# Kernel optimization log

Hardware: AMD Instinct MI355X
Metric: run time of the kernel (lower is better)

The kernel has to match this reference:

```python
import jax, jax.numpy as jnp
import numpy as np

N_SITES = 16
BATCH = 8192
K = 256
EPS = 1e-10


def _entanglement_entropy(sites_A, sites_B):
    # sites_A: [b, pA, k], sites_B: [b, pB, k]
    corr = jnp.einsum('bik,bjk->bij', sites_A, sites_B)  # [b, pA, pB]
    s = jnp.linalg.svd(corr, compute_uv=False)           # [b, min(pA,pB)]
    s_sq = s * s + EPS
    p = s_sq / jnp.sum(s_sq, axis=-1, keepdims=True)
    return -jnp.sum(p * jnp.log(p + EPS), axis=-1)        # [b]


def setup_inputs() -> dict:
    key = jax.random.key(0)
    sites = jax.random.normal(key, (BATCH, N_SITES, K), dtype=jnp.float32)
    return {"sites": sites}


def reference(sites) -> jnp.ndarray:
    # sites: [batch, n_sites, k]; list-of-tensors in the original, stacked here.
    n = sites.shape[1]
    mid = n // 2  # 8
    # Whole-system bipartition
    S_whole = _entanglement_entropy(sites[:, :mid], sites[:, mid:])
    # Left half bipartition (mid_left = mid // 2 = 4)
    ml = mid // 2
    S_left = _entanglement_entropy(sites[:, :ml], sites[:, ml:mid])
    # Right half bipartition
    nr = n - mid
    mr = nr // 2
    S_right = _entanglement_entropy(sites[:, mid:mid + mr], sites[:, mid + mr:])
    phi_q = S_whole - (S_left + S_right)
    return jax.nn.relu(phi_q)
```

## Files before the change

kernel.cpp:

```cpp
#include <hip/hip_runtime.h>
#include <math.h>

#define DEV __device__ __forceinline__

DEV float rcp_fast(float x) { return __builtin_amdgcn_rcpf(x); }
DEV float rsq_fast(float x) { return __builtin_amdgcn_rsqf(x); }

__host__ __device__ constexpr int TI(int n, int i, int j) {
  return n * i - (i * (i - 1)) / 2 + (j - i);
}

template <int N>
DEV float& sym_at(float (&a)[N * (N + 1) / 2], int i, int j) {
  return (i <= j) ? a[TI(N, i, j)] : a[TI(N, j, i)];
}

template <int N, int SWEEPS>
DEV void jacobi_sweeps(float (&a)[N * (N + 1) / 2]) {
  float tr = 0.0f;
#pragma unroll
  for (int i = 0; i < N; ++i) tr += a[TI(N, i, i)];
  const float thr = fabsf(tr) * 1e-8f + 1e-30f;
  for (int sw = 0; sw < SWEEPS; ++sw) {
#pragma unroll
    for (int p = 0; p < N - 1; ++p) {
#pragma unroll
      for (int q = p + 1; q < N; ++q) {
        float apq = a[TI(N, p, q)];
        if (fabsf(apq) > thr) {
          float app = a[TI(N, p, p)];
          float aqq = a[TI(N, q, q)];
          float h  = aqq - app;
          float tw = apq + apq;
          float den = fabsf(h) + sqrtf(fmaf(h, h, tw * tw));
          float t = tw * rcp_fast(den);
          t = (h < 0.0f) ? -t : t;
          float c = rsq_fast(fmaf(t, t, 1.0f));
          float s = t * c;
          float tau = s * rcp_fast(1.0f + c);
          a[TI(N, p, p)] = fmaf(-t, apq, app);
          a[TI(N, q, q)] = fmaf( t, apq, aqq);
          a[TI(N, p, q)] = 0.0f;
#pragma unroll
          for (int i = 0; i < N; ++i) {
            if (i != p && i != q) {
              float g  = sym_at<N>(a, i, p);
              float hh = sym_at<N>(a, i, q);
              sym_at<N>(a, i, p) = fmaf(-s, fmaf( tau, g, hh), g);
              sym_at<N>(a, i, q) = fmaf( s, fmaf(-tau, hh, g), hh);
            }
          }
        }
      }
    }
  }
}

template <int N>
DEV float entropy_of(const float (&a)[N * (N + 1) / 2]) {
  float lam[N];
  float sum = 0.0f;
#pragma unroll
  for (int i = 0; i < N; ++i) {
    float l = fmaxf(a[TI(N, i, i)], 0.0f) + 1e-10f;
    lam[i] = l;
    sum += l;
  }
  float inv = 1.0f / sum;
  float H = 0.0f;
#pragma unroll
  for (int i = 0; i < N; ++i) {
    float p = lam[i] * inv;
    H = fmaf(p, __logf(p + 1e-10f), H);
  }
  return -H;
}

DEV float reduce_dist_64(float (&cur)[64], int lane) {
#pragma unroll
  for (int d = 0; d < 6; ++d) {
    const int dist = 1 << d;
    const int up = (lane >> d) & 1;
#pragma unroll
    for (int m = 0; m < (64 >> (d + 1)); ++m) {
      float snd = up ? cur[2 * m]     : cur[2 * m + 1];
      float kp  = up ? cur[2 * m + 1] : cur[2 * m];
      float r = __shfl_xor(snd, dist, 64);
      cur[m] = kp + r;
    }
  }
  return cur[0];
}

DEV float reduce_dist_32(float (&cur)[32], int lane) {
#pragma unroll
  for (int d = 0; d < 5; ++d) {
    const int dist = 1 << d;
    const int up = (lane >> d) & 1;
#pragma unroll
    for (int m = 0; m < (32 >> (d + 1)); ++m) {
      float snd = up ? cur[2 * m]     : cur[2 * m + 1];
      float kp  = up ? cur[2 * m + 1] : cur[2 * m];
      float r = __shfl_xor(snd, dist, 64);
      cur[m] = kp + r;
    }
  }
  float v = cur[0];
  v += __shfl_xor(v, 32, 64);
  return v;
}

__global__ __launch_bounds__(64) void corr_kernel(
    const float* __restrict__ sites, float* __restrict__ cmat) {
  const int b = blockIdx.x;
  const int lane = threadIdx.x;
  const float4* base = reinterpret_cast<const float4*>(sites) + (size_t)b * 1024;

  float4 v[16];
#pragma unroll
  for (int s = 0; s < 16; ++s) v[s] = base[s * 64 + lane];

  float aw[64];
#pragma unroll
  for (int i = 0; i < 8; ++i) {
#pragma unroll
    for (int j = 0; j < 8; ++j) {
      float4 a = v[i], c = v[8 + j];
      aw[i * 8 + j] =
          fmaf(a.x, c.x, fmaf(a.y, c.y, fmaf(a.z, c.z, a.w * c.w)));
    }
  }
  float cw = reduce_dist_64(aw, lane);

  float alr[32];
#pragma unroll
  for (int i = 0; i < 4; ++i) {
#pragma unroll
    for (int j = 0; j < 4; ++j) {
      float4 a = v[i], c = v[4 + j];
      alr[i * 4 + j] =
          fmaf(a.x, c.x, fmaf(a.y, c.y, fmaf(a.z, c.z, a.w * c.w)));
      float4 a2 = v[8 + i], c2 = v[12 + j];
      alr[16 + i * 4 + j] =
          fmaf(a2.x, c2.x, fmaf(a2.y, c2.y, fmaf(a2.z, c2.z, a2.w * c2.w)));
    }
  }
  float clr = reduce_dist_32(alr, lane);

  cmat[(size_t)lane * 8192 + b] = cw;
  if (lane < 32) cmat[(size_t)(64 + lane) * 8192 + b] = clr;
}

__global__ __launch_bounds__(64) void phi_kernel(
    const float* __restrict__ cmat, float* __restrict__ out) {
  const int b = blockIdx.x * 64 + threadIdx.x;

  float Cw[64];
#pragma unroll
  for (int e = 0; e < 64; ++e) Cw[e] = cmat[(size_t)e * 8192 + b];
  float Mw[36];
#pragma unroll
  for (int i = 0; i < 8; ++i) {
#pragma unroll
    for (int j = i; j < 8; ++j) {
      float acc = 0.0f;
#pragma unroll
      for (int k = 0; k < 8; ++k) acc = fmaf(Cw[i * 8 + k], Cw[j * 8 + k], acc);
      Mw[TI(8, i, j)] = acc;
    }
  }
  jacobi_sweeps<8, 6>(Mw);
  float Sw = entropy_of<8>(Mw);

  float Cl[16];
#pragma unroll
  for (int e = 0; e < 16; ++e) Cl[e] = cmat[(size_t)(64 + e) * 8192 + b];
  float Ml[10];
#pragma unroll
  for (int i = 0; i < 4; ++i) {
#pragma unroll
    for (int j = i; j < 4; ++j) {
      float acc = 0.0f;
#pragma unroll
      for (int k = 0; k < 4; ++k) acc = fmaf(Cl[i * 4 + k], Cl[j * 4 + k], acc);
      Ml[TI(4, i, j)] = acc;
    }
  }
  jacobi_sweeps<4, 5>(Ml);
  float Sl = entropy_of<4>(Ml);

  float Cr[16];
#pragma unroll
  for (int e = 0; e < 16; ++e) Cr[e] = cmat[(size_t)(80 + e) * 8192 + b];
  float Mr[10];
#pragma unroll
  for (int i = 0; i < 4; ++i) {
#pragma unroll
    for (int j = i; j < 4; ++j) {
      float acc = 0.0f;
#pragma unroll
      for (int k = 0; k < 4; ++k) acc = fmaf(Cr[i * 4 + k], Cr[j * 4 + k], acc);
      Mr[TI(4, i, j)] = acc;
    }
  }
  jacobi_sweeps<4, 5>(Mr);
  float Sr = entropy_of<4>(Mr);

  out[b] = fmaxf(Sw - Sl - Sr, 0.0f);
}

extern "C" void kernel_launch(void* const* d_in, const int* in_sizes, int n_in,
                              void* d_out, int out_size, void* d_ws, size_t ws_size,
                              hipStream_t stream) {
  const float* sites = (const float*)d_in[0];
  float* out = (float*)d_out;
  float* cmat = (float*)d_ws;

  corr_kernel<<<8192, 64, 0, stream>>>(sites, cmat);
  phi_kernel<<<128, 64, 0, stream>>>(cmat, out);
}
```

Measured before the change: 219.9 us.

## Replace cyclic Jacobi with branch-free parallel-ordering Jacobi and interleave small eigensolves

Swaps the sequential cyclic Jacobi eigen-solver, with its per-pivot threshold branch, for a round-robin parallel ordering. Each round computes four (or two) independent rotations and then applies combined two-sided updates to the off-diagonal blocks, which gives more instruction-level parallelism and no divergence. The two 4x4 solves are interleaved and the sweep counts drop (6 to 5 and 5 to 4). This risks slightly less accurate eigenvalues, and without the threshold skip every rotation is always computed.

```diff
diff --git a/kernel.cpp b/kernel.cpp
--- a/kernel.cpp
+++ b/kernel.cpp
@@ -15,43 +15,81 @@
   return (i <= j) ? a[TI(N, i, j)] : a[TI(N, j, i)];
 }
 
-template <int N, int SWEEPS>
-DEV void jacobi_sweeps(float (&a)[N * (N + 1) / 2]) {
-  float tr = 0.0f;
-#pragma unroll
-  for (int i = 0; i < N; ++i) tr += a[TI(N, i, i)];
-  const float thr = fabsf(tr) * 1e-8f + 1e-30f;
+template <int N>
+DEV void pivot_params(float (&a)[N * (N + 1) / 2], int p, int q,
+                      float& c_out, float& s_out) {
+  float apq = a[TI(N, p, q)];
+  float app = a[TI(N, p, p)];
+  float aqq = a[TI(N, q, q)];
+  float h = aqq - app;
+  float tw = apq + apq;
+  float den = fabsf(h) + sqrtf(fmaf(h, h, tw * tw)) + 1e-37f;
+  float t = tw * rcp_fast(den);
+  t = (h < 0.0f) ? -t : t;
+  float c = rsq_fast(fmaf(t, t, 1.0f));
+  float s = t * c;
+  c_out = c;
+  s_out = s;
+  a[TI(N, p, p)] = fmaf(-t, apq, app);
+  a[TI(N, q, q)] = fmaf( t, apq, aqq);
+  a[TI(N, p, q)] = 0.0f;
+}
+
+template <int N>
+DEV void cross_update(float (&a)[N * (N + 1) / 2], int pa, int qa, int pb,
+                      int qb, float ca, float sa, float cb, float sb) {
+  float w = sym_at<N>(a, pa, pb), x = sym_at<N>(a, pa, qb);
+  float y = sym_at<N>(a, qa, pb), z = sym_at<N>(a, qa, qb);
+  float w1 = fmaf(ca, w, -sa * y), x1 = fmaf(ca, x, -sa * z);
+  float y1 = fmaf(sa, w,  ca * y), z1 = fmaf(sa, x,  ca * z);
+  sym_at<N>(a, pa, pb) = fmaf(cb, w1, -sb * x1);
+  sym_at<N>(a, pa, qb) = fmaf(sb, w1,  cb * x1);
+  sym_at<N>(a, qa, pb) = fmaf(cb, y1, -sb * z1);
+  sym_at<N>(a, qa, qb) = fmaf(sb, y1,  cb * z1);
+}
+
+template <int SWEEPS>
+DEV void pjacobi8(float (&a)[36]) {
+  constexpr int P[7][4][2] = {
+      {{0, 7}, {1, 6}, {2, 5}, {3, 4}}, {{0, 1}, {2, 7}, {3, 6}, {4, 5}},
+      {{0, 2}, {1, 3}, {4, 7}, {5, 6}}, {{0, 3}, {2, 4}, {1, 5}, {6, 7}},
+      {{0, 4}, {3, 5}, {2, 6}, {1, 7}}, {{0, 5}, {4, 6}, {3, 7}, {1, 2}},
+      {{0, 6}, {5, 7}, {1, 4}, {2, 3}}};
   for (int sw = 0; sw < SWEEPS; ++sw) {
 #pragma unroll
-    for (int p = 0; p < N - 1; ++p) {
-#pragma unroll
-      for (int q = p + 1; q < N; ++q) {
-        float apq = a[TI(N, p, q)];
-        if (fabsf(apq) > thr) {
-          float app = a[TI(N, p, p)];
-          float aqq = a[TI(N, q, q)];
-          float h  = aqq - app;
-          float tw = apq + apq;
-          float den = fabsf(h) + sqrtf(fmaf(h, h, tw * tw));
-          float t = tw * rcp_fast(den);
-          t = (h < 0.0f) ? -t : t;
-          float c = rsq_fast(fmaf(t, t, 1.0f));
-          float s = t * c;
-          float tau = s * rcp_fast(1.0f + c);
-          a[TI(N, p, p)] = fmaf(-t, apq, app);
-          a[TI(N, q, q)] = fmaf( t, apq, aqq);
-          a[TI(N, p, q)] = 0.0f;
-#pragma unroll
-          for (int i = 0; i < N; ++i) {
-            if (i != p && i != q) {
-              float g  = sym_at<N>(a, i, p);
-              float hh = sym_at<N>(a, i, q);
-              sym_at<N>(a, i, p) = fmaf(-s, fmaf( tau, g, hh), g);
-              sym_at<N>(a, i, q) = fmaf( s, fmaf(-tau, hh, g), hh);
-            }
-          }
+    for (int r = 0; r < 7; ++r) {
+      float cc[4], ss[4];
+#pragma unroll
+      for (int u = 0; u < 4; ++u)
+        pivot_params<8>(a, P[r][u][0], P[r][u][1], cc[u], ss[u]);
+#pragma unroll
+      for (int u = 0; u < 4; ++u) {
+#pragma unroll
+        for (int v = u + 1; v < 4; ++v) {
+          cross_update<8>(a, P[r][u][0], P[r][u][1], P[r][v][0], P[r][v][1],
+                          cc[u], ss[u], cc[v], ss[v]);
         }
       }
+    }
+  }
+}
+
+template <int SWEEPS>
+DEV void pjacobi4x2(float (&a)[10], float (&b)[10]) {
+  constexpr int P[3][2][2] = {
+      {{0, 3}, {1, 2}}, {{0, 1}, {2, 3}}, {{0, 2}, {1, 3}}};
+  for (int sw = 0; sw < SWEEPS; ++sw) {
+#pragma unroll
+    for (int r = 0; r < 3; ++r) {
+      float ca0, sa0, ca1, sa1, cb0, sb0, cb1, sb1;
+      pivot_params<4>(a, P[r][0][0], P[r][0][1], ca0, sa0);
+      pivot_params<4>(b, P[r][0][0], P[r][0][1], cb0, sb0);
+      pivot_params<4>(a, P[r][1][0], P[r][1][1], ca1, sa1);
+      pivot_params<4>(b, P[r][1][0], P[r][1][1], cb1, sb1);
+      cross_update<4>(a, P[r][0][0], P[r][0][1], P[r][1][0], P[r][1][1], ca0,
+                      sa0, ca1, sa1);
+      cross_update<4>(b, P[r][0][0], P[r][0][1], P[r][1][0], P[r][1][1], cb0,
+                      sb0, cb1, sb1);
     }
   }
 }
@@ -169,41 +207,33 @@
       Mw[TI(8, i, j)] = acc;
     }
   }
-  jacobi_sweeps<8, 6>(Mw);
+
+  float Cl[16], Cr[16];
+#pragma unroll
+  for (int e = 0; e < 16; ++e) Cl[e] = cmat[(size_t)(64 + e) * 8192 + b];
+#pragma unroll
+  for (int e = 0; e < 16; ++e) Cr[e] = cmat[(size_t)(80 + e) * 8192 + b];
+  float Ml[10], Mr[10];
+#pragma unroll
+  for (int i = 0; i < 4; ++i) {
+#pragma unroll
+    for (int j = i; j < 4; ++j) {
+      float accl = 0.0f, accr = 0.0f;
+#pragma unroll
+      for (int k = 0; k < 4; ++k) {
+        accl = fmaf(Cl[i * 4 + k], Cl[j * 4 + k], accl);
+        accr = fmaf(Cr[i * 4 + k], Cr[j * 4 + k], accr);
+      }
+      Ml[TI(4, i, j)] = accl;
+      Mr[TI(4, i, j)] = accr;
+    }
+  }
+
+  pjacobi8<5>(Mw);
+  pjacobi4x2<4>(Ml, Mr);
+
   float Sw = entropy_of<8>(Mw);
-
-  float Cl[16];
-#pragma unroll
-  for (int e = 0; e < 16; ++e) Cl[e] = cmat[(size_t)(64 + e) * 8192 + b];
-  float Ml[10];
-#pragma unroll
-  for (int i = 0; i < 4; ++i) {
-#pragma unroll
-    for (int j = i; j < 4; ++j) {
-      float acc = 0.0f;
-#pragma unroll
-      for (int k = 0; k < 4; ++k) acc = fmaf(Cl[i * 4 + k], Cl[j * 4 + k], acc);
-      Ml[TI(4, i, j)] = acc;
-    }
-  }
-  jacobi_sweeps<4, 5>(Ml);
   float Sl = entropy_of<4>(Ml);
-
-  float Cr[16];
-#pragma unroll
-  for (int e = 0; e < 16; ++e) Cr[e] = cmat[(size_t)(80 + e) * 8192 + b];
-  float Mr[10];
-#pragma unroll
-  for (int i = 0; i < 4; ++i) {
-#pragma unroll
-    for (int j = i; j < 4; ++j) {
-      float acc = 0.0f;
-#pragma unroll
-      for (int k = 0; k < 4; ++k) acc = fmaf(Cr[i * 4 + k], Cr[j * 4 + k], acc);
-      Mr[TI(4, i, j)] = acc;
-    }
-  }
-  jacobi_sweeps<4, 5>(Mr);
   float Sr = entropy_of<4>(Mr);
 
   out[b] = fmaxf(Sw - Sl - Sr, 0.0f);
```

New measurement: 212.9 us. 3.2% less time.
